# Kernel tuning notes

Measured on AMD Instinct MI355X. Metric: run time of the kernel, lower is better.

The kernel has to match this reference:

```python
import jax, jax.numpy as jnp
import numpy as np
import math

B, SEQ, PRED, NVAR, NMARK = 32, 512, 96, 862, 4
DM, DS, DFF, NL, DCONV = 512, 16, 512, 4, 2
DTR = math.ceil(DM / 16)  # mamba dt_rank = 32
EPS = 1e-5


def setup_inputs() -> dict:
    key = jax.random.key(0)
    ks = iter(jax.random.split(key, 48))
    rn = lambda shape, s=0.02: jax.random.normal(next(ks), shape, jnp.float32) * s
    inp = {
        "x_enc": jax.random.normal(next(ks), (B, SEQ, NVAR), jnp.float32),
        "x_mark_enc": jax.random.normal(next(ks), (B, SEQ, NMARK), jnp.float32),
        "x_dec": jax.random.normal(next(ks), (B, 144, NVAR), jnp.float32),
        "x_mark_dec": jax.random.normal(next(ks), (B, 144, NMARK), jnp.float32),
        # inverted embedding: Linear(seq_len -> d_model)
        "W_emb": rn((DM, SEQ)), "b_emb": jnp.zeros((DM,), jnp.float32),
        # per layer, 2 directional Mamba blocks (expand=1 -> d_inner = DM)
        "m_Win": rn((NL, 2, 2 * DM, DM)),
        "m_convw": rn((NL, 2, DM, DCONV), 0.2),
        "m_convb": jnp.zeros((NL, 2, DM), jnp.float32),
        "m_Wx": rn((NL, 2, DTR + 2 * DS, DM)),
        "m_Wdt": rn((NL, 2, DM, DTR), 0.1),
        "m_bdt": jnp.full((NL, 2, DM), -4.0, jnp.float32),
        "m_Alog": jnp.log(jnp.broadcast_to(jnp.arange(1, DS + 1, dtype=jnp.float32), (NL, 2, DM, DS))) + 0.0,
        "m_D": jnp.ones((NL, 2, DM), jnp.float32),
        "m_Wout": rn((NL, 2, DM, DM)),
        # position-wise FFN (Conv1d k=1 == Linear)
        "W1": rn((NL, DFF, DM)), "b1": jnp.zeros((NL, DFF), jnp.float32),
        "W2": rn((NL, DM, DFF)), "b2": jnp.zeros((NL, DM), jnp.float32),
        "ln1_g": jnp.ones((NL, DM), jnp.float32), "ln1_b": jnp.zeros((NL, DM), jnp.float32),
        "ln2_g": jnp.ones((NL, DM), jnp.float32), "ln2_b": jnp.zeros((NL, DM), jnp.float32),
        "lnf_g": jnp.ones((DM,), jnp.float32), "lnf_b": jnp.zeros((DM,), jnp.float32),
        "head_W": rn((PRED, DM)), "head_b": jnp.zeros((PRED,), jnp.float32),
        "train": 0,
    }
    return inp


def _ln(x, g, b):
    mu = x.mean(-1, keepdims=True)
    var = x.var(-1, keepdims=True)
    return (x - mu) * jax.lax.rsqrt(var + EPS) * g + b


def _mamba(u, Win, convw, convb, Wx, Wdt, bdt, Alog, Dp, Wout):
    # u: [B, L, DM] -> [B, L, DM]; selective scan (mamba_ssm semantics)
    Bsz, L, _ = u.shape
    xz = jnp.einsum('bld,ed->ble', u, Win)          # [B,L,2*DM]
    x, z = jnp.split(xz, 2, axis=-1)
    # depthwise causal conv, kernel size DCONV=2
    xp = jnp.pad(x, ((0, 0), (DCONV - 1, 0), (0, 0)))
    x = sum(xp[:, i:i + L] * convw[:, i] for i in range(DCONV)) + convb
    x = jax.nn.silu(x)
    dbc = jnp.einsum('bld,ed->ble', x, Wx)          # [B,L,DTR+2*DS]
    dt = jax.nn.softplus(jnp.einsum('blr,dr->bld', dbc[..., :DTR], Wdt) + bdt)  # [B,L,DM]
    Bm = dbc[..., DTR:DTR + DS]                      # [B,L,DS]
    Cm = dbc[..., DTR + DS:]                         # [B,L,DS]
    A = -jnp.exp(Alog)                               # [DM,DS]

    def step(h, inp):
        dt_t, B_t, C_t, x_t = inp                    # [B,DM],[B,DS],[B,DS],[B,DM]
        dA = jnp.exp(dt_t[..., None] * A)            # [B,DM,DS]
        h = dA * h + (dt_t * x_t)[..., None] * B_t[:, None, :]
        y = jnp.einsum('bds,bs->bd', h, C_t)
        return h, y

    h0 = jnp.zeros((Bsz, DM, DS), u.dtype)
    xs = (dt.transpose(1, 0, 2), Bm.transpose(1, 0, 2), Cm.transpose(1, 0, 2), x.transpose(1, 0, 2))
    _, ys = jax.lax.scan(step, h0, xs)               # ys: [L,B,DM]
    y = ys.transpose(1, 0, 2) + Dp * x
    y = y * jax.nn.silu(z)
    return jnp.einsum('bld,od->blo', y, Wout)


def _forward(x_enc, x_mark_enc, W_emb, b_emb, m_Win, m_convw, m_convb, m_Wx, m_Wdt,
             m_bdt, m_Alog, m_D, m_Wout, W1, b1, W2, b2, ln1_g, ln1_b, ln2_g, ln2_b,
             lnf_g, lnf_b, head_W, head_b):
    means = jax.lax.stop_gradient(x_enc.mean(1, keepdims=True))
    xc = x_enc - means
    stdev = jnp.sqrt(xc.var(1, keepdims=True) + EPS)   # unbiased=False
    xn = xc / stdev
    # inverted embedding: tokens = variates (+ time-mark channels)
    tok = jnp.concatenate([xn.transpose(0, 2, 1), x_mark_enc.transpose(0, 2, 1)], 1)  # [B, N+M, SEQ]
    h = jnp.einsum('bns,ds->bnd', tok, W_emb) + b_emb                                 # [B, N+M, DM]
    for l in range(NL):
        fwd = _mamba(h, m_Win[l, 0], m_convw[l, 0], m_convb[l, 0], m_Wx[l, 0],
                     m_Wdt[l, 0], m_bdt[l, 0], m_Alog[l, 0], m_D[l, 0], m_Wout[l, 0])
        rev = _mamba(h[:, ::-1], m_Win[l, 1], m_convw[l, 1], m_convb[l, 1], m_Wx[l, 1],
                     m_Wdt[l, 1], m_bdt[l, 1], m_Alog[l, 1], m_D[l, 1], m_Wout[l, 1])[:, ::-1]
        h = _ln(h + fwd + rev, ln1_g[l], ln1_b[l])
        y = jax.nn.gelu(jnp.einsum('bnd,fd->bnf', h, W1[l]) + b1[l], approximate=False)
        y = jnp.einsum('bnf,df->bnd', y, W2[l]) + b2[l]
        h = _ln(h + y, ln2_g[l], ln2_b[l])
    h = _ln(h, lnf_g, lnf_b)
    dec = jnp.einsum('bnd,pd->bnp', h, head_W) + head_b    # [B, N+M, PRED]
    dec = dec.transpose(0, 2, 1)[:, :, :NVAR]              # [B, PRED, N]
    dec = dec * stdev[:, 0:1, :] + means[:, 0:1, :]
    return dec[:, -PRED:, :]


def reference(x_enc, x_mark_enc, x_dec, x_mark_dec, W_emb, b_emb, m_Win, m_convw,
              m_convb, m_Wx, m_Wdt, m_bdt, m_Alog, m_D, m_Wout, W1, b1, W2, b2,
              ln1_g, ln1_b, ln2_g, ln2_b, lnf_g, lnf_b, head_W, head_b, train):
    dec = _forward(x_enc, x_mark_enc, W_emb, b_emb, m_Win, m_convw, m_convb, m_Wx,
                   m_Wdt, m_bdt, m_Alog, m_D, m_Wout, W1, b1, W2, b2, ln1_g, ln1_b,
                   ln2_g, ln2_b, lnf_g, lnf_b, head_W, head_b)
    loss_reg = jnp.float32(0.0)  # regularizer inactive in eval (train=False)
    return dec, loss_reg
```

## Files before the change

kernel.cpp:

```cpp
#include <hip/hip_runtime.h>
#include <hip/hip_bf16.h>
#include <cmath>

typedef __bf16 bf;
typedef __bf16 bfrag __attribute__((ext_vector_type(8)));
typedef __bf16 bf4 __attribute__((ext_vector_type(4)));
typedef float  f32x4 __attribute__((ext_vector_type(4)));

constexpr int BSZ = 32, SEQ = 512, NVAR = 862, NMARK = 4, NTOK = 866;
constexpr int DM = 512, DS = 16, DTR = 32, DFF = 512, NL = 4, PRED = 96;
constexpr int M = BSZ * NTOK;
constexpr float EPS = 1e-5f;
constexpr int NCH = 32, CL = 28;
static_assert(NCH * CL >= NTOK, "chunks must cover sequence");

__device__ __forceinline__ void gload16(const void* g, void* l) {
    __builtin_amdgcn_global_load_lds((const __attribute__((address_space(1))) void*)g,
                                     (__attribute__((address_space(3))) void*)l, 16, 0, 0);
}

__global__ void cvt_kernel(const float* __restrict__ src, bf* __restrict__ dst, int n4) {
    int i = blockIdx.x * 256 + threadIdx.x;
    if (i >= n4) return;
    f32x4 v = ((const f32x4*)src)[i];
    bf o[4];
    o[0] = (bf)v[0]; o[1] = (bf)v[1]; o[2] = (bf)v[2]; o[3] = (bf)v[3];
    *(uint2*)&dst[i * 4] = *(uint2*)o;
}

__global__ void fold_kernel(const float* __restrict__ Wdt, const float* __restrict__ Wx,
                            bf* __restrict__ out) {
    int idx = blockIdx.x * 256 + threadIdx.x;
    int k = idx & 511; int rest = idx >> 9;
    int row = rest % 544; int ld = rest / 544;
    float s;
    if (row < 512) {
        const float* wd = Wdt + ((size_t)ld * 512 + row) * 32;
        const float* wx = Wx + (size_t)ld * 64 * 512 + k;
        s = 0.f;
#pragma unroll 8
        for (int r = 0; r < 32; r++) s += wd[r] * wx[(size_t)r * 512];
    } else {
        s = Wx[(size_t)ld * 64 * 512 + (size_t)(32 + row - 512) * 512 + k];
    }
    out[((size_t)ld * 544 + row) * 512 + k] = (bf)s;
}

__global__ __launch_bounds__(256) void meanstd_kernel(const float* __restrict__ xe,
                               float* __restrict__ mean, float* __restrict__ stdv) {
    __shared__ float sm[2][4][64];
    int b = blockIdx.y;
    int vl = threadIdx.x & 63;
    int tg = threadIdx.x >> 6;
    int v = blockIdx.x * 64 + vl;
    float s = 0.f, sq = 0.f;
    if (v < NVAR) {
        const float* p = xe + (size_t)b * SEQ * NVAR + (size_t)tg * 128 * NVAR + v;
#pragma unroll 4
        for (int t = 0; t < 128; t++) {
            float x = p[(size_t)t * NVAR];
            s += x; sq += x * x;
        }
    }
    sm[0][tg][vl] = s; sm[1][tg][vl] = sq;
    __syncthreads();
    if (tg == 0 && v < NVAR) {
        s  = sm[0][0][vl] + sm[0][1][vl] + sm[0][2][vl] + sm[0][3][vl];
        sq = sm[1][0][vl] + sm[1][1][vl] + sm[1][2][vl] + sm[1][3][vl];
        float mu = s * (1.f / SEQ);
        float var = sq * (1.f / SEQ) - mu * mu;
        mean[b * NVAR + v] = mu;
        stdv[b * NVAR + v] = sqrtf(var + EPS);
    }
}

__global__ void tok_kernel(const float* __restrict__ xe, const float* __restrict__ xm,
                           const float* __restrict__ mean, const float* __restrict__ stdv,
                           bf* __restrict__ tok) {
    __shared__ float tile[32][33];
    int b = blockIdx.z;
    int v0 = blockIdx.x * 32, s0 = blockIdx.y * 32;
    int tx = threadIdx.x, ty = threadIdx.y;
    int v = v0 + tx;
    float mu = 0.f, rs = 0.f;
    if (v < NVAR) { mu = mean[b * NVAR + v]; rs = 1.f / stdv[b * NVAR + v]; }
#pragma unroll
    for (int j = 0; j < 4; j++) {
        int s = s0 + ty + j * 8;
        float val = 0.f;
        if (v < NVAR)       val = (xe[((size_t)b * SEQ + s) * NVAR + v] - mu) * rs;
        else if (v < NTOK)  val = xm[((size_t)b * SEQ + s) * NMARK + (v - NVAR)];
        tile[ty + j * 8][tx] = val;
    }
    __syncthreads();
#pragma unroll
    for (int j = 0; j < 4; j++) {
        int n = v0 + ty + j * 8;
        if (n < NTOK)
            tok[((size_t)b * NTOK + n) * SEQ + s0 + tx] = (bf)tile[tx][ty + j * 8];
    }
}

template <int BN, int ACT, bool BIAS, bool RES, bool HEAD, bool DTBC, typename CT>
__global__ __launch_bounds__(512, 4) void gemm_kernel(
    const bf* __restrict__ A0, const bf* __restrict__ A1,
    const bf* __restrict__ W0, const bf* __restrict__ W1,
    CT* __restrict__ C, float* __restrict__ C2,
    const float* __restrict__ bias, const bf* __restrict__ res,
    int Mreal, int Nreal, int K, int lda, int ldw, int ksplit, int ldc,
    size_t sAz, size_t sWz, size_t sCz, size_t sC2z, size_t sBiasz,
    const float* __restrict__ mean, const float* __restrict__ stdv) {
    constexpr int BM = 128, BK = 64;
    static_assert(BN == 128, "8-wave layout assumes 128x128 tile");
    constexpr int NT = 2;
    __shared__ __align__(16) bf Als[2][BM * BK];
    __shared__ __align__(16) bf Bls[2][BN * BK];

    int gx = gridDim.x, gy = gridDim.y;
    int gxy = gx * gy;
    int nbt = gxy * gridDim.z;
    int id = blockIdx.x + gx * (blockIdx.y + gy * blockIdx.z);
    int q8 = nbt >> 3, r8 = nbt & 7;
    int xcd = id & 7, rank = id >> 3;
    int w = xcd * q8 + (xcd < r8 ? xcd : r8) + rank;
    int z = w / gxy;
    int rem = w - z * gxy;
    int m0 = (rem / gy) * BM;
    int n0 = (rem % gy) * BN;

    A0 += (size_t)z * sAz; W0 += (size_t)z * sWz; C += (size_t)z * sCz;
    if (DTBC) C2 += (size_t)z * sC2z;
    if (BIAS) bias += (size_t)z * sBiasz;
    int tid = threadIdx.x, lane = tid & 63, wave = tid >> 6;
    int wm = wave >> 2, wn = wave & 3;
    int q = lane >> 4, ml = lane & 15;
    int srow = lane >> 3;
    int aswz = ((lane & 7) ^ srow) * 8;
    int swz = ((q ^ (ml & 7))) * 8;

    f32x4 acc[4][NT];
#pragma unroll
    for (int i = 0; i < 4; i++)
#pragma unroll
        for (int j = 0; j < NT; j++) { acc[i][j][0] = 0.f; acc[i][j][1] = 0.f; acc[i][j][2] = 0.f; acc[i][j][3] = 0.f; }

    auto stage = [&](int kt, int buf) {
        const bf* ab = (ksplit && kt >= ksplit) ? (A1 + (kt - ksplit)) : (A0 + kt);
        const bf* wb = (ksplit && kt >= ksplit) ? (W1 + (kt - ksplit)) : (W0 + kt);
#pragma unroll
        for (int i = 0; i < 2; i++) {
            int r = wave * 16 + i * 8;
            gload16(ab + (size_t)(m0 + r + srow) * lda + aswz, &Als[buf][r * BK]);
        }
#pragma unroll
        for (int i = 0; i < 2; i++) {
            int r = wave * 16 + i * 8;
            gload16(wb + (size_t)(n0 + r + srow) * ldw + aswz, &Bls[buf][r * BK]);
        }
    };

    stage(0, 0);
    int cur = 0;
    for (int kt = 0; kt < K; kt += BK) {
        bool pf = (kt + BK < K);
        if (pf) stage(kt + BK, cur ^ 1);
        if (pf) asm volatile("s_waitcnt vmcnt(4)" ::: "memory");
        else    asm volatile("s_waitcnt vmcnt(0)" ::: "memory");
        __builtin_amdgcn_s_barrier();
        __builtin_amdgcn_sched_barrier(0);
#pragma unroll
        for (int kk = 0; kk < BK; kk += 32) {
            bfrag af[4], bff[NT];
#pragma unroll
            for (int i = 0; i < 4; i++)
                af[i] = *(bfrag*)&Als[cur][(wm * 64 + i * 16 + ml) * BK + (swz ^ kk)];
#pragma unroll
            for (int j = 0; j < NT; j++)
                bff[j] = *(bfrag*)&Bls[cur][(wn * 32 + j * 16 + ml) * BK + (swz ^ kk)];
#pragma unroll
            for (int i = 0; i < 4; i++)
#pragma unroll
                for (int j = 0; j < NT; j++)
                    acc[i][j] = __builtin_amdgcn_mfma_f32_16x16x32_bf16(bff[j], af[i], acc[i][j], 0, 0, 0);
        }
        __builtin_amdgcn_sched_barrier(0);
        __builtin_amdgcn_s_barrier();
        cur ^= 1;
    }

#pragma unroll
    for (int i = 0; i < 4; i++) {
        int row = m0 + wm * 64 + i * 16 + ml;
        if (row >= Mreal) continue;
#pragma unroll
        for (int j = 0; j < NT; j++) {
            int colb = n0 + wn * 32 + j * 16 + q * 4;
            if (colb >= Nreal) continue;
            f32x4 x = acc[i][j];
            if constexpr (BIAS) {
                if (!DTBC || colb < 512) {
                    f32x4 bv = *(const f32x4*)&bias[colb];
#pragma unroll
                    for (int r = 0; r < 4; r++) x[r] += bv[r];
                }
            }
            if constexpr (DTBC) {
                if (colb < 512) {
#pragma unroll
                    for (int r = 0; r < 4; r++)
                        x[r] = (x[r] > 20.f) ? x[r] : __logf(1.f + __expf(x[r]));
                    *(f32x4*)&C[(size_t)row * 512 + colb] = x;
                } else {
                    *(f32x4*)&C2[(size_t)row * 32 + (colb - 512)] = x;
                }
            } else {
                if constexpr (ACT == 1) {
#pragma unroll
                    for (int r = 0; r < 4; r++)
                        x[r] = 0.5f * x[r] * (1.f + erff(x[r] * 0.70710678118654752f));
                }
                if constexpr (RES) {
                    bf4 rv = *(const bf4*)&res[(size_t)row * DM + colb];
#pragma unroll
                    for (int r = 0; r < 4; r++) x[r] += (float)rv[r];
                }
                if constexpr (HEAD) {
                    int bidx = row / NTOK, n = row - bidx * NTOK;
                    if (n < NVAR) {
                        float sc = stdv[bidx * NVAR + n], mm = mean[bidx * NVAR + n];
#pragma unroll
                        for (int r = 0; r < 4; r++) {
                            int col = colb + r;
                            if (col < Nreal)
                                C[((size_t)bidx * PRED + col) * NVAR + n] = (CT)(x[r] * sc + mm);
                        }
                    }
                } else {
                    bf4 ov;
#pragma unroll
                    for (int r = 0; r < 4; r++) ov[r] = (bf)x[r];
                    *(bf4*)&C[(size_t)row * ldc + colb] = ov;
                }
            }
        }
    }
    if (HEAD && blockIdx.x == 0 && blockIdx.y == 0 && blockIdx.z == 0 && tid == 0)
        C[(size_t)BSZ * PRED * NVAR] = (CT)0.f;
}

__global__ void conv_kernel(const bf* __restrict__ xz, const float* __restrict__ cw,
                            const float* __restrict__ cb, bf* __restrict__ xc, int Mc) {
    int id = blockIdx.x * 256 + threadIdx.x;
    int dir = id / (Mc * 64); int rem = id - dir * (Mc * 64);
    int token = rem >> 6; int ch0 = (rem & 63) * 8;
    int t = token % NTOK;
    const bf* xb = xz + (size_t)token * (4 * DM) + dir * (2 * DM) + ch0;
    bfrag xt = *(const bfrag*)xb;
    bfrag xn;
#pragma unroll
    for (int i = 0; i < 8; i++) xn[i] = (bf)0.f;
    int tn = dir ? t + 1 : t - 1;
    if ((unsigned)tn < (unsigned)NTOK)
        xn = *(const bfrag*)(xb + (dir ? (4 * DM) : -(4 * DM)));
    const float2* cwp = (const float2*)cw + ((size_t)dir * DM + ch0);
    const float*  cbp = cb + (size_t)dir * DM + ch0;
    bfrag ov;
#pragma unroll
    for (int jj = 0; jj < 8; jj++) {
        float2 w = cwp[jj];
        float x = (float)xn[jj] * w.x + (float)xt[jj] * w.y + cbp[jj];
        x = x / (1.f + __expf(-x));
        ov[jj] = (bf)x;
    }
    *(bfrag*)(xc + (size_t)dir * Mc * DM + (size_t)token * DM + ch0) = ov;
}

template <bool FINAL>
__global__ __launch_bounds__(64) void scan_chunk_kernel(
    const float* __restrict__ dtc, const float* __restrict__ dbc,
    const bf* __restrict__ xc, const bf* __restrict__ xz,
    const float* __restrict__ Alog, const float* __restrict__ Dp,
    float* __restrict__ hloc, float* __restrict__ aprod,
    bf* __restrict__ y, int Mc) {
    __shared__ __align__(16) float row[32];
    int lane = threadIdx.x;
    int dg = blockIdx.x, b = blockIdx.y;
    int zc = blockIdx.z; int dir = zc / NCH, c = zc - dir * NCH;
    int d = dg * 64 + lane;
    int dd = dir * DM + d;
    float A2[16];
    {
        const f32x4* ap = (const f32x4*)(Alog + (size_t)dd * DS);
#pragma unroll
        for (int i = 0; i < 4; i++) {
            f32x4 v = ap[i];
#pragma unroll
            for (int jj = 0; jj < 4; jj++)
                A2[i * 4 + jj] = -__expf(v[jj]) * 1.4426950408889634f;
        }
    }
    float A20 = A2[0];
    bool lc = true;
#pragma unroll
    for (int s = 1; s < 16; s++)
        lc = lc && (fabsf(A2[s] - (s + 1) * A20) <= 1e-4f * fabsf(A2[s]));
    bool fast = (__ballot(lc) == ~0ull);
    float Dd = FINAL ? Dp[dd] : 0.f;

    const size_t sbase = (((((size_t)b * 2 + dir) * 8 + dg) * NCH + c) * 16) * 64 + lane;
    float h[16];
#pragma unroll
    for (int s = 0; s < 16; s++) h[s] = FINAL ? hloc[sbase + (size_t)s * 64] : 0.f;
    float dtsum = 0.f;

    const int t0 = c * CL;
    const int t1e = (t0 + CL < NTOK) ? t0 + CL : NTOK;
    const long step = dir ? -1 : 1;

    const float* dtp = nullptr; const float* bcp = nullptr;
    const bf* xcp = nullptr; const bf* xzp = nullptr; bf* yp = nullptr;
    float dtq = 0.f; f32x4 gq = {0.f, 0.f, 0.f, 0.f}; bf xq = (bf)0.f, zq = (bf)0.f;
    if (t0 < t1e) {
        long tok0 = (long)b * NTOK + (dir ? (NTOK - 1 - t0) : t0);
        dtp = dtc + (size_t)dir * Mc * 512 + (size_t)tok0 * 512 + d;
        bcp = dbc + ((size_t)dir * Mc + (size_t)tok0) * 32;
        xcp = xc + (size_t)dir * Mc * 512 + (size_t)tok0 * 512 + d;
        dtq = *dtp;
        if (lane < 8) gq = ((const f32x4*)bcp)[lane];
        xq = *xcp;
        if (FINAL) {
            xzp = xz + (size_t)tok0 * 2048 + dir * 1024 + 512 + d;
            yp  = y  + (size_t)tok0 * 1024 + dir * 512 + d;
            zq = *xzp;
        }
    }
    const long sdt = step * 512, sbc = step * 32, sxc = step * 512;
    const long sxz = step * 2048, sy = step * 1024;

    for (int t = t0; t < t1e; t++) {
        if (lane < 8) ((f32x4*)row)[lane] = gq;
        float dt = dtq;
        float x = (float)xq;
        float zv = (float)zq;
        bf* ypc = yp;
        if (t + 1 < t1e) {
            dtp += sdt; bcp += sbc; xcp += sxc;
            dtq = *dtp;
            if (lane < 8) gq = ((const f32x4*)bcp)[lane];
            xq = *xcp;
            if (FINAL) { xzp += sxz; zq = *xzp; yp += sy; }
        }
        const f32x4* rv = (const f32x4*)row;
        float dtx = dt * x;
        dtsum += dt;
        float yv = 0.f;
        if (fast) {
            float r = exp2f(dt * A20);
            float rp = 1.f;
#pragma unroll
            for (int i = 0; i < 4; i++) {
                f32x4 Bv = rv[i];
                f32x4 Cv = rv[4 + i];
#pragma unroll
                for (int jj = 0; jj < 4; jj++) {
                    int s = i * 4 + jj;
                    rp *= r;
                    h[s] = rp * h[s] + dtx * Bv[jj];
                    if (FINAL) yv += Cv[jj] * h[s];
                }
            }
        } else {
#pragma unroll
            for (int i = 0; i < 4; i++) {
                f32x4 Bv = rv[i];
                f32x4 Cv = rv[4 + i];
#pragma unroll
                for (int jj = 0; jj < 4; jj++) {
                    int s = i * 4 + jj;
                    float a = exp2f(dt * A2[s]);
                    h[s] = a * h[s] + dtx * Bv[jj];
                    if (FINAL) yv += Cv[jj] * h[s];
                }
            }
        }
        if (FINAL) {
            float sz = zv / (1.f + __expf(-zv));
            *ypc = (bf)((yv + Dd * x) * sz);
        }
    }
    if (!FINAL) {
#pragma unroll
        for (int s = 0; s < 16; s++) {
            hloc[sbase + (size_t)s * 64] = h[s];
            aprod[sbase + (size_t)s * 64] = exp2f(dtsum * A2[s]);
        }
    }
}

__global__ void scan_fix_kernel(float* __restrict__ hloc, const float* __restrict__ aprod, int total) {
    int tid = blockIdx.x * 256 + threadIdx.x;
    if (tid >= total) return;
    int lane = tid & 63;
    int s = (tid >> 6) & 15;
    int g = tid >> 10;
    size_t i0 = (((size_t)g * NCH) * 16 + s) * 64 + lane;
    float H = 0.f;
#pragma unroll
    for (int c = 0; c < NCH; c++) {
        size_t ix = i0 + (size_t)c * 1024;
        float hl = hloc[ix];
        float ap = aprod[ix];
        hloc[ix] = H;
        H = hl + ap * H;
    }
}

__global__ __launch_bounds__(256) void ln_kernel(const bf* X, bf* Y,
                                                 const float* __restrict__ g, const float* __restrict__ bb) {
    int token = blockIdx.x * 4 + (threadIdx.x >> 6);
    int lane = threadIdx.x & 63;
    bfrag xv = *(const bfrag*)(X + (size_t)token * DM + lane * 8);
    float xf[8]; float s = 0.f, sq = 0.f;
#pragma unroll
    for (int j = 0; j < 8; j++) { xf[j] = (float)xv[j]; s += xf[j]; sq += xf[j] * xf[j]; }
#pragma unroll
    for (int o = 1; o < 64; o <<= 1) { s += __shfl_xor(s, o); sq += __shfl_xor(sq, o); }
    float mu = s * (1.f / DM);
    float rs = rsqrtf(sq * (1.f / DM) - mu * mu + EPS);
    f32x4 g0 = ((const f32x4*)g)[lane * 2], g1 = ((const f32x4*)g)[lane * 2 + 1];
    f32x4 b0 = ((const f32x4*)bb)[lane * 2], b1 = ((const f32x4*)bb)[lane * 2 + 1];
    bfrag ov;
#pragma unroll
    for (int j = 0; j < 8; j++) {
        float gg = (j < 4) ? g0[j] : g1[j - 4];
        float bbv = (j < 4) ? b0[j] : b1[j - 4];
        ov[j] = (bf)((xf[j] - mu) * rs * gg + bbv);
    }
    *(bfrag*)(Y + (size_t)token * DM + lane * 8) = ov;
}

extern "C" void kernel_launch(void* const* d_in, const int* in_sizes, int n_in,
                              void* d_out, int out_size, void* d_ws, size_t ws_size,
                              hipStream_t stream) {
    const float* x_enc = (const float*)d_in[0];
    const float* x_mark = (const float*)d_in[1];
    const float* W_emb = (const float*)d_in[4];
    const float* b_emb = (const float*)d_in[5];
    const float* mWin = (const float*)d_in[6];
    const float* mcw = (const float*)d_in[7];
    const float* mcb = (const float*)d_in[8];
    const float* mWx = (const float*)d_in[9];
    const float* mWdt = (const float*)d_in[10];
    const float* mbdt = (const float*)d_in[11];
    const float* mAlog = (const float*)d_in[12];
    const float* mD = (const float*)d_in[13];
    const float* mWout = (const float*)d_in[14];
    const float* W1w = (const float*)d_in[15];
    const float* b1w = (const float*)d_in[16];
    const float* W2w = (const float*)d_in[17];
    const float* b2w = (const float*)d_in[18];
    const float* ln1g = (const float*)d_in[19];
    const float* ln1b = (const float*)d_in[20];
    const float* ln2g = (const float*)d_in[21];
    const float* ln2b = (const float*)d_in[22];
    const float* lnfg = (const float*)d_in[23];
    const float* lnfb = (const float*)d_in[24];
    const float* headW = (const float*)d_in[25];
    const float* headb = (const float*)d_in[26];

    auto a256 = [](size_t x) { return (x + 255) & ~(size_t)255; };
    char* ws = (char*)d_ws;
    size_t off = 0;
    auto alloc = [&](size_t n) { size_t r = off; off += a256(n); return ws + r; };
    float* mean = (float*)alloc((size_t)BSZ * NVAR * 4);
    float* stdv = (float*)alloc((size_t)BSZ * NVAR * 4);
    bf* h  = (bf*)alloc((size_t)M * DM * 2);
    bf* t1 = (bf*)alloc((size_t)M * DM * 2);
    bf* t2 = (bf*)alloc((size_t)M * DM * 2);
    constexpr int nEmb = 512 * 512, nWin = NL * 2 * 1024 * 512,
                  nWout = NL * 2 * 512 * 512, nW1 = NL * DFF * DM, nW2 = NL * DM * DFF,
                  nHead = PRED * DM, nComb = NL * 2 * 544 * 512;
    bf* wEmb  = (bf*)alloc((size_t)nEmb * 2);
    bf* wWin  = (bf*)alloc((size_t)nWin * 2);
    bf* wWout = (bf*)alloc((size_t)nWout * 2);
    bf* wW1   = (bf*)alloc((size_t)nW1 * 2);
    bf* wW2   = (bf*)alloc((size_t)nW2 * 2);
    bf* wHead = (bf*)alloc((size_t)nHead * 2);
    bf* wComb = (bf*)alloc((size_t)nComb * 2);
    size_t fixedEnd = off;

    auto scanScr = [&](size_t cb) { return cb * 2 * 8 * (size_t)NCH * 16 * 64 * 4; };
    int CB = 1;
    {
        int cbs[6] = {32, 16, 8, 4, 2, 1};
        for (int i = 0; i < 6; i++) {
            size_t mc = (size_t)cbs[i] * NTOK;
            size_t chunkB = a256(mc * 4096) + a256(mc * 2048) + a256(mc * 256)
                          + a256(mc * 2048) + a256(mc * 4096) + 2 * a256(scanScr(cbs[i]));
            if (fixedEnd + chunkB <= ws_size) { CB = cbs[i]; break; }
        }
    }
    const size_t Mc = (size_t)CB * NTOK;
    size_t co = fixedEnd;
    bf* xzc = (bf*)(ws + co);        co += a256(Mc * 4096);
    bf* xcc = (bf*)(ws + co);        co += a256(Mc * 2048);
    float* dbcc = (float*)(ws + co); co += a256(Mc * 256);
    bf* ycc = (bf*)(ws + co);        co += a256(Mc * 2048);
    float* dtcc = (float*)(ws + co); co += a256(Mc * 4096);
    float* hloc = (float*)(ws + co); co += a256(scanScr(CB));
    float* aprod = (float*)(ws + co);
    const int NC = BSZ / CB;
    const int MTc = (int)((Mc + 127) / 128);
    constexpr int MT = (M + 127) / 128;
    const int fixTotal = CB * 2 * 8 * 16 * 64;

    cvt_kernel<<<(nEmb / 4 + 255) / 256, 256, 0, stream>>>(W_emb, wEmb, nEmb / 4);
    cvt_kernel<<<(nWin / 4 + 255) / 256, 256, 0, stream>>>(mWin, wWin, nWin / 4);
    cvt_kernel<<<(nWout / 4 + 255) / 256, 256, 0, stream>>>(mWout, wWout, nWout / 4);
    cvt_kernel<<<(nW1 / 4 + 255) / 256, 256, 0, stream>>>(W1w, wW1, nW1 / 4);
    cvt_kernel<<<(nW2 / 4 + 255) / 256, 256, 0, stream>>>(W2w, wW2, nW2 / 4);
    cvt_kernel<<<(nHead / 4 + 255) / 256, 256, 0, stream>>>(headW, wHead, nHead / 4);
    fold_kernel<<<(nComb + 255) / 256, 256, 0, stream>>>(mWdt, mWx, wComb);

    meanstd_kernel<<<dim3(14, BSZ), 256, 0, stream>>>(x_enc, mean, stdv);
    tok_kernel<<<dim3(28, 16, BSZ), dim3(32, 8), 0, stream>>>(x_enc, x_mark, mean, stdv, t1);
    gemm_kernel<128, 0, true, false, false, false, bf><<<dim3(MT, 4), 512, 0, stream>>>(
        t1, nullptr, wEmb, nullptr, h, nullptr, b_emb, nullptr,
        M, DM, SEQ, SEQ, SEQ, 0, DM, 0, 0, 0, 0, 0, nullptr, nullptr);

    for (int l = 0; l < NL; l++) {
        const bf* Winl = wWin + (size_t)l * 2 * 1024 * 512;
        const float* cwl = mcw + (size_t)l * 2 * DM * 2;
        const float* cbl = mcb + (size_t)l * 2 * DM;
        const bf* Combl = wComb + (size_t)l * 2 * 544 * 512;
        const float* bdtl = mbdt + (size_t)l * 2 * DM;
        const float* Alogl = mAlog + (size_t)l * 2 * 512 * 16;
        const float* Dl = mD + (size_t)l * 2 * DM;
        const bf* Woutl = wWout + (size_t)l * 2 * 512 * 512;
        const bf* W1l = wW1 + (size_t)l * DFF * DM;
        const bf* W2l = wW2 + (size_t)l * DM * DFF;

        for (int c = 0; c < NC; c++) {
            size_t coff = (size_t)c * Mc;
            gemm_kernel<128, 0, false, false, false, false, bf><<<dim3(MTc, 16), 512, 0, stream>>>(
                h + coff * DM, nullptr, Winl, nullptr, xzc, nullptr, nullptr, nullptr,
                (int)Mc, 2048, 512, 512, 512, 0, 2048, 0, 0, 0, 0, 0, nullptr, nullptr);
            conv_kernel<<<(int)(2 * Mc * 64 / 256), 256, 0, stream>>>(xzc, cwl, cbl, xcc, (int)Mc);
            gemm_kernel<128, 0, true, false, false, true, float><<<dim3(MTc, 5, 2), 512, 0, stream>>>(
                xcc, nullptr, Combl, nullptr, dtcc, dbcc, bdtl, nullptr,
                (int)Mc, 544, 512, 512, 512, 0, 512,
                Mc * 512, (size_t)544 * 512, Mc * 512, Mc * 32, 512, nullptr, nullptr);
            scan_chunk_kernel<false><<<dim3(8, CB, 2 * NCH), 64, 0, stream>>>(
                dtcc, dbcc, xcc, xzc, Alogl, Dl, hloc, aprod, ycc, (int)Mc);
            scan_fix_kernel<<<(fixTotal + 255) / 256, 256, 0, stream>>>(hloc, aprod, fixTotal);
            scan_chunk_kernel<true><<<dim3(8, CB, 2 * NCH), 64, 0, stream>>>(
                dtcc, dbcc, xcc, xzc, Alogl, Dl, hloc, aprod, ycc, (int)Mc);
            gemm_kernel<128, 0, false, true, false, false, bf><<<dim3(MTc, 4), 512, 0, stream>>>(
                ycc, ycc + 512, Woutl, Woutl + 512 * 512, t1 + coff * DM, nullptr, nullptr, h + coff * DM,
                (int)Mc, DM, 1024, 1024, 512, 512, DM, 0, 0, 0, 0, 0, nullptr, nullptr);
        }
        ln_kernel<<<M / 4, 256, 0, stream>>>(t1, t2, ln1g + l * DM, ln1b + l * DM);
        gemm_kernel<128, 1, true, false, false, false, bf><<<dim3(MT, 4), 512, 0, stream>>>(
            t2, nullptr, W1l, nullptr, t1, nullptr, b1w + l * DFF, nullptr,
            M, DFF, DM, DM, DM, 0, DFF, 0, 0, 0, 0, 0, nullptr, nullptr);
        gemm_kernel<128, 0, true, true, false, false, bf><<<dim3(MT, 4), 512, 0, stream>>>(
            t1, nullptr, W2l, nullptr, h, nullptr, b2w + l * DM, t2,
            M, DM, DFF, DFF, DFF, 0, DM, 0, 0, 0, 0, 0, nullptr, nullptr);
        ln_kernel<<<M / 4, 256, 0, stream>>>(h, h, ln2g + l * DM, ln2b + l * DM);
    }

    ln_kernel<<<M / 4, 256, 0, stream>>>(h, t1, lnfg, lnfb);
    gemm_kernel<128, 0, true, false, true, false, float><<<dim3(MT, 1), 512, 0, stream>>>(
        t1, nullptr, wHead, nullptr, (float*)d_out, nullptr, headb, nullptr,
        M, PRED, DM, DM, DM, 0, 1, 0, 0, 0, 0, 0, mean, stdv);
}
```

Baseline: 3.124 ms.

## Store dt in fp16 and recompute chunk decay from dt sums in fix pass

The softplus dt output of the projection GEMM is now written as fp16 instead of fp32, which halves the dt traffic read by both scan passes. The chunk-scan pass no longer writes a per-state decay product array. It writes one dt sum per channel, and the fix kernel recomputes exp2(dtsum*A) from Alog. This cuts scratch writes and reads by roughly 16x for that array and shrinks workspace, at the cost of fp16 precision on dt and extra exp work in the fix kernel.

```diff
diff --git a/kernel.cpp b/kernel.cpp
--- a/kernel.cpp
+++ b/kernel.cpp
@@ -3,8 +3,10 @@
 #include <cmath>
 
 typedef __bf16 bf;
+typedef _Float16 fp16;
 typedef __bf16 bfrag __attribute__((ext_vector_type(8)));
 typedef __bf16 bf4 __attribute__((ext_vector_type(4)));
+typedef _Float16 h4 __attribute__((ext_vector_type(4)));
 typedef float  f32x4 __attribute__((ext_vector_type(4)));
 
 constexpr int BSZ = 32, SEQ = 512, NVAR = 862, NMARK = 4, NTOK = 866;
@@ -206,10 +208,13 @@
             }
             if constexpr (DTBC) {
                 if (colb < 512) {
-#pragma unroll
-                    for (int r = 0; r < 4; r++)
-                        x[r] = (x[r] > 20.f) ? x[r] : __logf(1.f + __expf(x[r]));
-                    *(f32x4*)&C[(size_t)row * 512 + colb] = x;
+                    h4 hv;
+#pragma unroll
+                    for (int r = 0; r < 4; r++) {
+                        float xs = (x[r] > 20.f) ? x[r] : __logf(1.f + __expf(x[r]));
+                        hv[r] = (_Float16)xs;
+                    }
+                    *(h4*)&C[(size_t)row * 512 + colb] = hv;
                 } else {
                     *(f32x4*)&C2[(size_t)row * 32 + (colb - 512)] = x;
                 }
@@ -277,10 +282,10 @@
 
 template <bool FINAL>
 __global__ __launch_bounds__(64) void scan_chunk_kernel(
-    const float* __restrict__ dtc, const float* __restrict__ dbc,
+    const fp16* __restrict__ dtc, const float* __restrict__ dbc,
     const bf* __restrict__ xc, const bf* __restrict__ xz,
     const float* __restrict__ Alog, const float* __restrict__ Dp,
-    float* __restrict__ hloc, float* __restrict__ aprod,
+    float* __restrict__ hloc, float* __restrict__ dtsums,
     bf* __restrict__ y, int Mc) {
     __shared__ __align__(16) float row[32];
     int lane = threadIdx.x;
@@ -307,7 +312,8 @@
     bool fast = (__ballot(lc) == ~0ull);
     float Dd = FINAL ? Dp[dd] : 0.f;
 
-    const size_t sbase = (((((size_t)b * 2 + dir) * 8 + dg) * NCH + c) * 16) * 64 + lane;
+    const size_t gbase = ((((size_t)b * 2 + dir) * 8 + dg) * NCH + c);
+    const size_t sbase = gbase * 1024 + lane;
     float h[16];
 #pragma unroll
     for (int s = 0; s < 16; s++) h[s] = FINAL ? hloc[sbase + (size_t)s * 64] : 0.f;
@@ -317,7 +323,7 @@
     const int t1e = (t0 + CL < NTOK) ? t0 + CL : NTOK;
     const long step = dir ? -1 : 1;
 
-    const float* dtp = nullptr; const float* bcp = nullptr;
+    const fp16* dtp = nullptr; const float* bcp = nullptr;
     const bf* xcp = nullptr; const bf* xzp = nullptr; bf* yp = nullptr;
     float dtq = 0.f; f32x4 gq = {0.f, 0.f, 0.f, 0.f}; bf xq = (bf)0.f, zq = (bf)0.f;
     if (t0 < t1e) {
@@ -325,7 +331,7 @@
         dtp = dtc + (size_t)dir * Mc * 512 + (size_t)tok0 * 512 + d;
         bcp = dbc + ((size_t)dir * Mc + (size_t)tok0) * 32;
         xcp = xc + (size_t)dir * Mc * 512 + (size_t)tok0 * 512 + d;
-        dtq = *dtp;
+        dtq = (float)*dtp;
         if (lane < 8) gq = ((const f32x4*)bcp)[lane];
         xq = *xcp;
         if (FINAL) {
@@ -345,7 +351,7 @@
         bf* ypc = yp;
         if (t + 1 < t1e) {
             dtp += sdt; bcp += sbc; xcp += sxc;
-            dtq = *dtp;
+            dtq = (float)*dtp;
             if (lane < 8) gq = ((const f32x4*)bcp)[lane];
             xq = *xcp;
             if (FINAL) { xzp += sxz; zq = *xzp; yp += sy; }
@@ -390,26 +396,29 @@
     }
     if (!FINAL) {
 #pragma unroll
-        for (int s = 0; s < 16; s++) {
-            hloc[sbase + (size_t)s * 64] = h[s];
-            aprod[sbase + (size_t)s * 64] = exp2f(dtsum * A2[s]);
-        }
-    }
-}
-
-__global__ void scan_fix_kernel(float* __restrict__ hloc, const float* __restrict__ aprod, int total) {
+        for (int s = 0; s < 16; s++) hloc[sbase + (size_t)s * 64] = h[s];
+        dtsums[gbase * 64 + lane] = dtsum;
+    }
+}
+
+__global__ void scan_fix_kernel(float* __restrict__ hloc, const float* __restrict__ dtsums,
+                                const float* __restrict__ Alog, int total) {
     int tid = blockIdx.x * 256 + threadIdx.x;
     if (tid >= total) return;
     int lane = tid & 63;
     int s = (tid >> 6) & 15;
     int g = tid >> 10;
+    int dg = g & 7, dir = (g >> 3) & 1;
+    int dd = dir * DM + dg * 64 + lane;
+    float A2s = -__expf(Alog[(size_t)dd * DS + s]) * 1.4426950408889634f;
     size_t i0 = (((size_t)g * NCH) * 16 + s) * 64 + lane;
+    size_t d0 = ((size_t)g * NCH) * 64 + lane;
     float H = 0.f;
 #pragma unroll
     for (int c = 0; c < NCH; c++) {
         size_t ix = i0 + (size_t)c * 1024;
         float hl = hloc[ix];
-        float ap = aprod[ix];
+        float ap = exp2f(dtsums[d0 + (size_t)c * 64] * A2s);
         hloc[ix] = H;
         H = hl + ap * H;
     }
@@ -490,13 +499,15 @@
     size_t fixedEnd = off;
 
     auto scanScr = [&](size_t cb) { return cb * 2 * 8 * (size_t)NCH * 16 * 64 * 4; };
+    auto dtsScr  = [&](size_t cb) { return cb * 2 * 8 * (size_t)NCH * 64 * 4; };
     int CB = 1;
     {
         int cbs[6] = {32, 16, 8, 4, 2, 1};
         for (int i = 0; i < 6; i++) {
             size_t mc = (size_t)cbs[i] * NTOK;
             size_t chunkB = a256(mc * 4096) + a256(mc * 2048) + a256(mc * 256)
-                          + a256(mc * 2048) + a256(mc * 4096) + 2 * a256(scanScr(cbs[i]));
+                          + a256(mc * 2048) + a256(mc * 2048)
+                          + a256(scanScr(cbs[i])) + a256(dtsScr(cbs[i]));
             if (fixedEnd + chunkB <= ws_size) { CB = cbs[i]; break; }
         }
     }
@@ -506,9 +517,9 @@
     bf* xcc = (bf*)(ws + co);        co += a256(Mc * 2048);
     float* dbcc = (float*)(ws + co); co += a256(Mc * 256);
     bf* ycc = (bf*)(ws + co);        co += a256(Mc * 2048);
-    float* dtcc = (float*)(ws + co); co += a256(Mc * 4096);
+    fp16* dtcc = (fp16*)(ws + co);   co += a256(Mc * 2048);
     float* hloc = (float*)(ws + co); co += a256(scanScr(CB));
-    float* aprod = (float*)(ws + co);
+    float* dtsums = (float*)(ws + co);
     const int NC = BSZ / CB;
     const int MTc = (int)((Mc + 127) / 128);
     constexpr int MT = (M + 127) / 128;
@@ -546,15 +557,15 @@
                 h + coff * DM, nullptr, Winl, nullptr, xzc, nullptr, nullptr, nullptr,
                 (int)Mc, 2048, 512, 512, 512, 0, 2048, 0, 0, 0, 0, 0, nullptr, nullptr);
             conv_kernel<<<(int)(2 * Mc * 64 / 256), 256, 0, stream>>>(xzc, cwl, cbl, xcc, (int)Mc);
-            gemm_kernel<128, 0, true, false, false, true, float><<<dim3(MTc, 5, 2), 512, 0, stream>>>(
+            gemm_kernel<128, 0, true, false, false, true, _Float16><<<dim3(MTc, 5, 2), 512, 0, stream>>>(
                 xcc, nullptr, Combl, nullptr, dtcc, dbcc, bdtl, nullptr,
                 (int)Mc, 544, 512, 512, 512, 0, 512,
                 Mc * 512, (size_t)544 * 512, Mc * 512, Mc * 32, 512, nullptr, nullptr);
             scan_chunk_kernel<false><<<dim3(8, CB, 2 * NCH), 64, 0, stream>>>(
-                dtcc, dbcc, xcc, xzc, Alogl, Dl, hloc, aprod, ycc, (int)Mc);
-            scan_fix_kernel<<<(fixTotal + 255) / 256, 256, 0, stream>>>(hloc, aprod, fixTotal);
+                dtcc, dbcc, xcc, xzc, Alogl, Dl, hloc, dtsums, ycc, (int)Mc);
+            scan_fix_kernel<<<(fixTotal + 255) / 256, 256, 0, stream>>>(hloc, dtsums, Alogl, fixTotal);
             scan_chunk_kernel<true><<<dim3(8, CB, 2 * NCH), 64, 0, stream>>>(
-                dtcc, dbcc, xcc, xzc, Alogl, Dl, hloc, aprod, ycc, (int)Mc);
+                dtcc, dbcc, xcc, xzc, Alogl, Dl, hloc, dtsums, ycc, (int)Mc);
             gemm_kernel<128, 0, false, true, false, false, bf><<<dim3(MTc, 4), 512, 0, stream>>>(
                 ycc, ycc + 512, Woutl, Woutl + 512 * 512, t1 + coff * DM, nullptr, nullptr, h + coff * DM,
                 (int)Mc, DM, 1024, 1024, 512, 512, DM, 0, 0, 0, 0, 0, nullptr, nullptr);
```

Measured after the change: 2.942 ms. 5.8% less time.
